# Kernel optimization log

Measured on AMD Instinct MI355X. Metric: run time of the kernel, lower is better.

## Reference

```python
import jax, jax.numpy as jnp
from jax import lax
import numpy as np

S = 2        # scale_factor
K = 5        # upsample_kernel_size
M = 64       # m_channels
C_IN = 128

def setup_inputs() -> dict:
    key = jax.random.key(0)
    k1, k2, k3, k4, k5 = jax.random.split(key, 5)
    B, C, H, W = 8, C_IN, 64, 64
    x = jax.random.normal(k1, (B, C, H, W), dtype=jnp.float32)
    compress_w = jax.random.normal(k2, (M, C, 1, 1), dtype=jnp.float32) * 0.05
    compress_b = jax.random.normal(k3, (M,), dtype=jnp.float32) * 0.05
    n_out = K * K * S * S  # 100
    encoder_w = jax.random.normal(k4, (n_out, M, 3, 3), dtype=jnp.float32) * 0.05
    encoder_b = jax.random.normal(k5, (n_out,), dtype=jnp.float32) * 0.05
    return {"x": x, "compress_w": compress_w, "compress_b": compress_b,
            "encoder_w": encoder_w, "encoder_b": encoder_b}

def _carafe(x, compress_w, compress_b, encoder_w, encoder_b):
    B, C, H, W = x.shape
    k, s = K, S
    nH, nW = s * H, s * W
    # 1x1 compress conv
    m = jnp.einsum('bchw,mc->bmhw', x, compress_w[:, :, 0, 0]) + compress_b[None, :, None, None]
    # 3x3 encoder conv, stride 1, pad 1 (SAME)
    ker = lax.conv_general_dilated(m, encoder_w, window_strides=(1, 1), padding='SAME',
                                   dimension_numbers=('NCHW', 'OIHW', 'NCHW'))
    ker = ker + encoder_b[None, :, None, None]  # (B, k*k*s*s, H, W)
    # PixelShuffle(s): (B, k*k, s, s, H, W) -> (B, k*k, H, s, W, s) -> (B, k*k, nH, nW)
    ker = ker.reshape(B, k * k, s, s, H, W).transpose(0, 1, 4, 2, 5, 3).reshape(B, k * k, nH, nW)
    ker = jax.nn.softmax(ker, axis=1)
    # Unfold(k, stride=1, pad=k//2): stack k*k shifted views, ordering (kh outer, kw inner)
    pad = k // 2
    xp = jnp.pad(x, ((0, 0), (0, 0), (pad, pad), (pad, pad)))
    patches = jnp.stack([xp[:, :, i:i + H, j:j + W] for i in range(k) for j in range(k)],
                        axis=2)  # (B, C, k*k, H, W)
    # nearest upsample by s on spatial dims
    up = jnp.repeat(jnp.repeat(patches, s, axis=3), s, axis=4)  # (B, C, k*k, nH, nW)
    # weighted local sum
    out = jnp.sum(up * ker[:, None, :, :, :], axis=2)  # (B, C, nH, nW)
    return out

def reference(x, compress_w, compress_b, encoder_w, encoder_b):
    return _carafe(x, compress_w, compress_b, encoder_w, encoder_b)
```

## Files before the change

### kernel.cpp

```cpp
#include <hip/hip_runtime.h>
#include <math.h>


typedef __attribute__((ext_vector_type(8))) short short8;
typedef __attribute__((ext_vector_type(4))) float floatx4;
typedef __attribute__((ext_vector_type(2))) float v2f;

__device__ __forceinline__ unsigned short f2bf(float f) {
  union { float f; unsigned int u; } v; v.f = f;
  unsigned int u = v.u + 0x7fffu + ((v.u >> 16) & 1u);
  return (unsigned short)(u >> 16);
}
__device__ __forceinline__ void unpack2(unsigned int u, float& lo, float& hi) {
  union { unsigned int u; float f; } a, b;
  a.u = u << 16; b.u = u & 0xffff0000u;
  lo = a.f; hi = b.f;
}
__device__ __forceinline__ v2f unpack2v(unsigned int u) {
  union { unsigned int u; float f; } a, b;
  a.u = u << 16; b.u = u & 0xffff0000u;
  return (v2f){a.f, b.f};
}

__global__ __launch_bounds__(256) void k_prep_pad(
    const float* __restrict__ x, const float* __restrict__ ew,
    const float* __restrict__ cw, unsigned short* __restrict__ a_prep,
    float* __restrict__ cwT, unsigned short* __restrict__ xpad) {
  const int blk = blockIdx.x;
  if (blk < 1024) {
    const float* xs = x + (size_t)blk * 4096;
    unsigned short* xd = xpad + (size_t)blk * 4896;
    for (int idx = threadIdx.x; idx < 1224; idx += 256) {
      int hp = idx / 18;
      int q = idx - hp * 18;
      int hh = hp - 2;
      int w0 = q * 4 - 2;
      float v0, v1, v2, v3;
      if (hh >= 0 && hh < 64 && w0 >= 0 && w0 + 3 < 64) {
        float4 xv = *(const float4*)&xs[hh * 64 + w0];
        v0 = xv.x; v1 = xv.y; v2 = xv.z; v3 = xv.w;
      } else {
        int base = hh * 64;
        bool hok = (hh >= 0 && hh < 64);
        v0 = (hok && w0 + 0 >= 0 && w0 + 0 < 64) ? xs[base + w0 + 0] : 0.f;
        v1 = (hok && w0 + 1 >= 0 && w0 + 1 < 64) ? xs[base + w0 + 1] : 0.f;
        v2 = (hok && w0 + 2 >= 0 && w0 + 2 < 64) ? xs[base + w0 + 2] : 0.f;
        v3 = (hok && w0 + 3 >= 0 && w0 + 3 < 64) ? xs[base + w0 + 3] : 0.f;
      }
      ushort4 o;
      o.x = f2bf(v0); o.y = f2bf(v1); o.z = f2bf(v2); o.w = f2bf(v3);
      *(ushort4*)&xd[idx * 4] = o;
    }
  } else {
    int idx = (blk - 1024) * 256 + (int)threadIdx.x;
    if (idx < 9 * 128 * 64) {
      int mo = idx & 63;
      int n = (idx >> 6) & 127;
      int tap = idx >> 13;
      float v = (n < 100) ? ew[(n * 64 + mo) * 9 + tap] : 0.f;
      a_prep[idx] = f2bf(v);
    } else {
      int r = idx - 9 * 128 * 64;
      int c = r >> 6, mo = r & 63;
      cwT[c * 64 + mo] = cw[mo * 128 + c];
    }
  }
}

__global__ __launch_bounds__(256) void k_compress(
    const float* __restrict__ x, const float* __restrict__ cwT,
    const float* __restrict__ cb, unsigned short* __restrict__ m_t) {
  __shared__ __align__(16) unsigned short ms[64][72];
  const int b = blockIdx.x >> 6;
  const int h = blockIdx.x & 63;
  const int wv = __builtin_amdgcn_readfirstlane((int)(threadIdx.x >> 6));
  const int lane = (int)(threadIdx.x & 63);
  const int mo0 = wv * 16;

  float acc[16];
#pragma unroll
  for (int k = 0; k < 16; ++k) acc[k] = 0.f;

  const float* xp = x + (((size_t)b * 128) * 64 + h) * 64 + lane;
  const float* wp = cwT + mo0;

#pragma unroll 4
  for (int c = 0; c < 128; ++c) {
    float xv = xp[(size_t)c * 4096];
#pragma unroll
    for (int k = 0; k < 16; ++k)
      acc[k] = fmaf(xv, wp[c * 64 + k], acc[k]);
  }

#pragma unroll
  for (int k = 0; k < 16; ++k) acc[k] += cb[mo0 + k];

#pragma unroll
  for (int k = 0; k < 8; ++k) {
    unsigned int p = ((unsigned int)f2bf(acc[2 * k + 1]) << 16) | f2bf(acc[2 * k]);
    *(unsigned int*)&ms[lane][mo0 + 2 * k] = p;
  }
  __syncthreads();
  const int t = threadIdx.x;
#pragma unroll
  for (int rep = 0; rep < 2; ++rep) {
    int idx = t + rep * 256;
    uint4 v = *(const uint4*)&ms[idx >> 3][(idx & 7) * 8];
    *(uint4*)&m_t[(size_t)blockIdx.x * 4096 + idx * 8] = v;
  }
}

__global__ __launch_bounds__(256) void k_main(
    const unsigned short* __restrict__ m_t, const unsigned short* __restrict__ a_prep,
    const float* __restrict__ eb, const unsigned short* __restrict__ xpad,
    float* __restrict__ out) {
  __shared__ __align__(16) float raw[128 * 66];
  unsigned short* m_s = (unsigned short*)raw;
  unsigned short* wgt_s = (unsigned short*)raw;
  const int b = blockIdx.x >> 6;
  const int h = blockIdx.x & 63;
  const int t = threadIdx.x;

  for (int idx = t; idx < 3 * 64 * 8; idx += 256) {
    int r = idx >> 9;
    int rem = idx & 511;
    int w = rem >> 3, u = rem & 7;
    int hh = h + r - 1;
    uint4 val = make_uint4(0u, 0u, 0u, 0u);
    if (hh >= 0 && hh < 64)
      val = *(const uint4*)&m_t[(((b * 64 + hh) * 64 + w) * 64) + u * 8];
    *(uint4*)&m_s[(r * 64 + w) * 72 + u * 8] = val;
  }
  __syncthreads();

  const int wave = t >> 6, lane = t & 63;
  const int quad = lane >> 4, col = lane & 15;
  const int nbase = wave * 32;

  const floatx4 z4 = {0.f, 0.f, 0.f, 0.f};
  floatx4 acc[2][4];
#pragma unroll
  for (int i = 0; i < 2; ++i)
#pragma unroll
    for (int p = 0; p < 4; ++p) acc[i][p] = z4;

  const short8 z8 = {0, 0, 0, 0, 0, 0, 0, 0};

#pragma unroll
  for (int tap = 0; tap < 9; ++tap) {
    const int dh = tap / 3, dw = tap % 3;
#pragma unroll
    for (int half = 0; half < 2; ++half) {
      const int mo0 = half * 32;
      short8 a0 = *(const short8*)&a_prep[((tap * 128 + nbase + col) * 64) + mo0 + quad * 8];
      short8 a1 = *(const short8*)&a_prep[((tap * 128 + nbase + 16 + col) * 64) + mo0 + quad * 8];
#pragma unroll
      for (int p = 0; p < 4; ++p) {
        int wsrc = p * 16 + col + dw - 1;
        int wc = min(max(wsrc, 0), 63);
        short8 bf = *(const short8*)&m_s[(dh * 64 + wc) * 72 + mo0 + quad * 8];
        if (wsrc < 0 || wsrc > 63) bf = z8;
        acc[0][p] = __builtin_amdgcn_mfma_f32_16x16x32_bf16(a0, bf, acc[0][p], 0, 0, 0);
        acc[1][p] = __builtin_amdgcn_mfma_f32_16x16x32_bf16(a1, bf, acc[1][p], 0, 0, 0);
      }
    }
  }

  __syncthreads();
#pragma unroll
  for (int i = 0; i < 2; ++i)
#pragma unroll
    for (int p = 0; p < 4; ++p)
#pragma unroll
      for (int r = 0; r < 4; ++r)
        raw[(nbase + i * 16 + quad * 4 + r) * 66 + p * 16 + col] = acc[i][p][r];
  __syncthreads();

  const int q = wave;
  float v[25];
  float mx = -1e30f;
#pragma unroll
  for (int kk = 0; kk < 25; ++kk) {
    v[kk] = raw[(kk * 4 + q) * 66 + lane] + eb[kk * 4 + q];
    mx = fmaxf(mx, v[kk]);
  }
  float s = 0.f;
#pragma unroll
  for (int kk = 0; kk < 25; ++kk) {
    v[kk] = __expf(v[kk] - mx);
    s += v[kk];
  }
  float inv = 1.f / s;

  __syncthreads();
  {
    const int ohl = q >> 1;
    const int owp = 2 * lane + (q & 1);
#pragma unroll
    for (int kk = 0; kk < 25; ++kk)
      wgt_s[(ohl * 25 + kk) * 128 + owp] = f2bf(v[kk] * inv);
  }
  __syncthreads();

  const int wg = t & 15;
  const int cg = t >> 4;
  const int w0 = wg * 4;

  for (int chalf = 0; chalf < 2; ++chalf) {
    const int c0 = chalf * 64 + cg * 4;
    const unsigned short* xb =
        xpad + ((size_t)(b * 128 + c0) * 4896) + h * 72 + w0;

    v2f accB[2][4][4];
#pragma unroll
    for (int oh = 0; oh < 2; ++oh)
#pragma unroll
      for (int ch = 0; ch < 4; ++ch)
#pragma unroll
        for (int k = 0; k < 4; ++k) accB[oh][ch][k] = (v2f){0.f, 0.f};

    for (int i = 0; i < 5; ++i) {
      float xr[4][8];
#pragma unroll
      for (int ch = 0; ch < 4; ++ch) {
        uint4 rawv = *(const uint4*)(xb + ch * 4896 + i * 72);
        unpack2(rawv.x, xr[ch][0], xr[ch][1]);
        unpack2(rawv.y, xr[ch][2], xr[ch][3]);
        unpack2(rawv.z, xr[ch][4], xr[ch][5]);
        unpack2(rawv.w, xr[ch][6], xr[ch][7]);
      }
#pragma unroll
      for (int j = 0; j < 5; ++j) {
        const int ij = i * 5 + j;
#pragma unroll
        for (int oh = 0; oh < 2; ++oh) {
          uint4 wr = *(const uint4*)&wgt_s[(oh * 25 + ij) * 128 + w0 * 2];
          v2f wp[4];
          wp[0] = unpack2v(wr.x);
          wp[1] = unpack2v(wr.y);
          wp[2] = unpack2v(wr.z);
          wp[3] = unpack2v(wr.w);
#pragma unroll
          for (int k = 0; k < 4; ++k)
#pragma unroll
            for (int ch = 0; ch < 4; ++ch) {
              float xv = xr[ch][k + j];
              v2f xvv = {xv, xv};
              accB[oh][ch][k] += xvv * wp[k];
            }
        }
      }
    }

#pragma unroll
    for (int ch = 0; ch < 4; ++ch)
#pragma unroll
      for (int oh = 0; oh < 2; ++oh) {
        float* orow =
            out + ((size_t)(b * 128 + c0 + ch) * 128 + (2 * h + oh)) * 128 + w0 * 2;
        float4 f0 = make_float4(accB[oh][ch][0].x, accB[oh][ch][0].y,
                                accB[oh][ch][1].x, accB[oh][ch][1].y);
        float4 f1 = make_float4(accB[oh][ch][2].x, accB[oh][ch][2].y,
                                accB[oh][ch][3].x, accB[oh][ch][3].y);
        *(float4*)orow = f0;
        *(float4*)(orow + 4) = f1;
      }
  }
}

extern "C" void kernel_launch(void* const* d_in, const int* in_sizes, int n_in,
                              void* d_out, int out_size, void* d_ws, size_t ws_size,
                              hipStream_t stream) {
  (void)in_sizes; (void)n_in; (void)out_size; (void)ws_size;
  const float* x  = (const float*)d_in[0];
  const float* cw = (const float*)d_in[1];
  const float* cb = (const float*)d_in[2];
  const float* ew = (const float*)d_in[3];
  const float* eb = (const float*)d_in[4];
  float* out = (float*)d_out;

  char* wsb = (char*)d_ws;
  unsigned short* m_t    = (unsigned short*)(wsb);
  unsigned short* a_prep = (unsigned short*)(wsb + 4194304);
  unsigned short* xpad   = (unsigned short*)(wsb + 4341760);
  float*          cwT    = (float*)(wsb + 14368768);

  k_prep_pad<<<dim3(1344), dim3(256), 0, stream>>>(x, ew, cw, a_prep, cwT, xpad);
  k_compress<<<dim3(512), dim3(256), 0, stream>>>(x, cwT, cb, m_t);
  k_main<<<dim3(512), dim3(256), 0, stream>>>(m_t, a_prep, eb, xpad, out);
}
```

Before: 145.4 us.

## Fuse bf16 padded-x write into compress kernel and widen main kernel to 512 threads

```diff
diff --git a/kernel.cpp b/kernel.cpp
--- a/kernel.cpp
+++ b/kernel.cpp
@@ -23,36 +23,15 @@
 }
 
 __global__ __launch_bounds__(256) void k_prep_pad(
-    const float* __restrict__ x, const float* __restrict__ ew,
-    const float* __restrict__ cw, unsigned short* __restrict__ a_prep,
-    float* __restrict__ cwT, unsigned short* __restrict__ xpad) {
+    const float* __restrict__ ew, const float* __restrict__ cw,
+    unsigned short* __restrict__ a_prep, float* __restrict__ cwT,
+    unsigned short* __restrict__ xpad) {
   const int blk = blockIdx.x;
-  if (blk < 1024) {
-    const float* xs = x + (size_t)blk * 4096;
-    unsigned short* xd = xpad + (size_t)blk * 4896;
-    for (int idx = threadIdx.x; idx < 1224; idx += 256) {
-      int hp = idx / 18;
-      int q = idx - hp * 18;
-      int hh = hp - 2;
-      int w0 = q * 4 - 2;
-      float v0, v1, v2, v3;
-      if (hh >= 0 && hh < 64 && w0 >= 0 && w0 + 3 < 64) {
-        float4 xv = *(const float4*)&xs[hh * 64 + w0];
-        v0 = xv.x; v1 = xv.y; v2 = xv.z; v3 = xv.w;
-      } else {
-        int base = hh * 64;
-        bool hok = (hh >= 0 && hh < 64);
-        v0 = (hok && w0 + 0 >= 0 && w0 + 0 < 64) ? xs[base + w0 + 0] : 0.f;
-        v1 = (hok && w0 + 1 >= 0 && w0 + 1 < 64) ? xs[base + w0 + 1] : 0.f;
-        v2 = (hok && w0 + 2 >= 0 && w0 + 2 < 64) ? xs[base + w0 + 2] : 0.f;
-        v3 = (hok && w0 + 3 >= 0 && w0 + 3 < 64) ? xs[base + w0 + 3] : 0.f;
-      }
-      ushort4 o;
-      o.x = f2bf(v0); o.y = f2bf(v1); o.z = f2bf(v2); o.w = f2bf(v3);
-      *(ushort4*)&xd[idx * 4] = o;
-    }
+  if (blk < 2448) {
+    int idx = blk * 256 + (int)threadIdx.x;
+    *(uint4*)&xpad[(size_t)idx * 8] = make_uint4(0u, 0u, 0u, 0u);
   } else {
-    int idx = (blk - 1024) * 256 + (int)threadIdx.x;
+    int idx = (blk - 2448) * 256 + (int)threadIdx.x;
     if (idx < 9 * 128 * 64) {
       int mo = idx & 63;
       int n = (idx >> 6) & 127;
@@ -69,7 +48,8 @@
 
 __global__ __launch_bounds__(256) void k_compress(
     const float* __restrict__ x, const float* __restrict__ cwT,
-    const float* __restrict__ cb, unsigned short* __restrict__ m_t) {
+    const float* __restrict__ cb, unsigned short* __restrict__ m_t,
+    unsigned short* __restrict__ xpad) {
   __shared__ __align__(16) unsigned short ms[64][72];
   const int b = blockIdx.x >> 6;
   const int h = blockIdx.x & 63;
@@ -83,10 +63,14 @@
 
   const float* xp = x + (((size_t)b * 128) * 64 + h) * 64 + lane;
   const float* wp = cwT + mo0;
+  unsigned short* xpd =
+      xpad + ((size_t)(b * 128) * 4896) + (h + 2) * 72 + 2 + lane;
 
 #pragma unroll 4
   for (int c = 0; c < 128; ++c) {
     float xv = xp[(size_t)c * 4096];
+    if ((c >> 5) == wv)
+      xpd[(size_t)c * 4896] = f2bf(xv);
 #pragma unroll
     for (int k = 0; k < 16; ++k)
       acc[k] = fmaf(xv, wp[c * 64 + k], acc[k]);
@@ -110,7 +94,7 @@
   }
 }
 
-__global__ __launch_bounds__(256) void k_main(
+__global__ __launch_bounds__(512, 4) void k_main(
     const unsigned short* __restrict__ m_t, const unsigned short* __restrict__ a_prep,
     const float* __restrict__ eb, const unsigned short* __restrict__ xpad,
     float* __restrict__ out) {
@@ -121,7 +105,7 @@
   const int h = blockIdx.x & 63;
   const int t = threadIdx.x;
 
-  for (int idx = t; idx < 3 * 64 * 8; idx += 256) {
+  for (int idx = t; idx < 3 * 64 * 8; idx += 512) {
     int r = idx >> 9;
     int rem = idx & 511;
     int w = rem >> 3, u = rem & 7;
@@ -135,14 +119,12 @@
 
   const int wave = t >> 6, lane = t & 63;
   const int quad = lane >> 4, col = lane & 15;
-  const int nbase = wave * 32;
+  const int nbase = wave * 16;
 
   const floatx4 z4 = {0.f, 0.f, 0.f, 0.f};
-  floatx4 acc[2][4];
-#pragma unroll
-  for (int i = 0; i < 2; ++i)
-#pragma unroll
-    for (int p = 0; p < 4; ++p) acc[i][p] = z4;
+  floatx4 acc[4];
+#pragma unroll
+  for (int p = 0; p < 4; ++p) acc[p] = z4;
 
   const short8 z8 = {0, 0, 0, 0, 0, 0, 0, 0};
 
@@ -153,47 +135,46 @@
     for (int half = 0; half < 2; ++half) {
       const int mo0 = half * 32;
       short8 a0 = *(const short8*)&a_prep[((tap * 128 + nbase + col) * 64) + mo0 + quad * 8];
-      short8 a1 = *(const short8*)&a_prep[((tap * 128 + nbase + 16 + col) * 64) + mo0 + quad * 8];
 #pragma unroll
       for (int p = 0; p < 4; ++p) {
         int wsrc = p * 16 + col + dw - 1;
         int wc = min(max(wsrc, 0), 63);
         short8 bf = *(const short8*)&m_s[(dh * 64 + wc) * 72 + mo0 + quad * 8];
         if (wsrc < 0 || wsrc > 63) bf = z8;
-        acc[0][p] = __builtin_amdgcn_mfma_f32_16x16x32_bf16(a0, bf, acc[0][p], 0, 0, 0);
-        acc[1][p] = __builtin_amdgcn_mfma_f32_16x16x32_bf16(a1, bf, acc[1][p], 0, 0, 0);
+        acc[p] = __builtin_amdgcn_mfma_f32_16x16x32_bf16(a0, bf, acc[p], 0, 0, 0);
       }
     }
   }
 
   __syncthreads();
 #pragma unroll
-  for (int i = 0; i < 2; ++i)
-#pragma unroll
-    for (int p = 0; p < 4; ++p)
-#pragma unroll
-      for (int r = 0; r < 4; ++r)
-        raw[(nbase + i * 16 + quad * 4 + r) * 66 + p * 16 + col] = acc[i][p][r];
-  __syncthreads();
-
-  const int q = wave;
+  for (int p = 0; p < 4; ++p)
+#pragma unroll
+    for (int r = 0; r < 4; ++r)
+      raw[(nbase + quad * 4 + r) * 66 + p * 16 + col] = acc[p][r];
+  __syncthreads();
+
   float v[25];
-  float mx = -1e30f;
-#pragma unroll
-  for (int kk = 0; kk < 25; ++kk) {
-    v[kk] = raw[(kk * 4 + q) * 66 + lane] + eb[kk * 4 + q];
-    mx = fmaxf(mx, v[kk]);
-  }
-  float s = 0.f;
-#pragma unroll
-  for (int kk = 0; kk < 25; ++kk) {
-    v[kk] = __expf(v[kk] - mx);
-    s += v[kk];
-  }
-  float inv = 1.f / s;
-
-  __syncthreads();
-  {
+  float inv = 0.f;
+  if (t < 256) {
+    const int q = wave;
+    float mx = -1e30f;
+#pragma unroll
+    for (int kk = 0; kk < 25; ++kk) {
+      v[kk] = raw[(kk * 4 + q) * 66 + lane] + eb[kk * 4 + q];
+      mx = fmaxf(mx, v[kk]);
+    }
+    float s = 0.f;
+#pragma unroll
+    for (int kk = 0; kk < 25; ++kk) {
+      v[kk] = __expf(v[kk] - mx);
+      s += v[kk];
+    }
+    inv = 1.f / s;
+  }
+  __syncthreads();
+  if (t < 256) {
+    const int q = wave;
     const int ohl = q >> 1;
     const int owp = 2 * lane + (q & 1);
 #pragma unroll
@@ -205,67 +186,65 @@
   const int wg = t & 15;
   const int cg = t >> 4;
   const int w0 = wg * 4;
-
-  for (int chalf = 0; chalf < 2; ++chalf) {
-    const int c0 = chalf * 64 + cg * 4;
-    const unsigned short* xb =
-        xpad + ((size_t)(b * 128 + c0) * 4896) + h * 72 + w0;
-
-    v2f accB[2][4][4];
-#pragma unroll
-    for (int oh = 0; oh < 2; ++oh)
-#pragma unroll
-      for (int ch = 0; ch < 4; ++ch)
-#pragma unroll
-        for (int k = 0; k < 4; ++k) accB[oh][ch][k] = (v2f){0.f, 0.f};
-
-    for (int i = 0; i < 5; ++i) {
-      float xr[4][8];
-#pragma unroll
-      for (int ch = 0; ch < 4; ++ch) {
-        uint4 rawv = *(const uint4*)(xb + ch * 4896 + i * 72);
-        unpack2(rawv.x, xr[ch][0], xr[ch][1]);
-        unpack2(rawv.y, xr[ch][2], xr[ch][3]);
-        unpack2(rawv.z, xr[ch][4], xr[ch][5]);
-        unpack2(rawv.w, xr[ch][6], xr[ch][7]);
+  const int c0 = cg * 4;
+
+  const unsigned short* xb =
+      xpad + ((size_t)(b * 128 + c0) * 4896) + h * 72 + w0;
+
+  v2f accB[2][4][4];
+#pragma unroll
+  for (int oh = 0; oh < 2; ++oh)
+#pragma unroll
+    for (int ch = 0; ch < 4; ++ch)
+#pragma unroll
+      for (int k = 0; k < 4; ++k) accB[oh][ch][k] = (v2f){0.f, 0.f};
+
+  for (int i = 0; i < 5; ++i) {
+    float xr[4][8];
+#pragma unroll
+    for (int ch = 0; ch < 4; ++ch) {
+      uint4 rawv = *(const uint4*)(xb + ch * 4896 + i * 72);
+      unpack2(rawv.x, xr[ch][0], xr[ch][1]);
+      unpack2(rawv.y, xr[ch][2], xr[ch][3]);
+      unpack2(rawv.z, xr[ch][4], xr[ch][5]);
+      unpack2(rawv.w, xr[ch][6], xr[ch][7]);
+    }
+#pragma unroll
+    for (int j = 0; j < 5; ++j) {
+      const int ij = i * 5 + j;
+#pragma unroll
+      for (int oh = 0; oh < 2; ++oh) {
+        uint4 wr = *(const uint4*)&wgt_s[(oh * 25 + ij) * 128 + w0 * 2];
+        v2f wp[4];
+        wp[0] = unpack2v(wr.x);
+        wp[1] = unpack2v(wr.y);
+        wp[2] = unpack2v(wr.z);
+        wp[3] = unpack2v(wr.w);
+#pragma unroll
+        for (int k = 0; k < 4; ++k)
+#pragma unroll
+          for (int ch = 0; ch < 4; ++ch) {
+            float xv = xr[ch][k + j];
+            v2f xvv = {xv, xv};
+            accB[oh][ch][k] += xvv * wp[k];
+          }
       }
-#pragma unroll
-      for (int j = 0; j < 5; ++j) {
-        const int ij = i * 5 + j;
-#pragma unroll
-        for (int oh = 0; oh < 2; ++oh) {
-          uint4 wr = *(const uint4*)&wgt_s[(oh * 25 + ij) * 128 + w0 * 2];
-          v2f wp[4];
-          wp[0] = unpack2v(wr.x);
-          wp[1] = unpack2v(wr.y);
-          wp[2] = unpack2v(wr.z);
-          wp[3] = unpack2v(wr.w);
-#pragma unroll
-          for (int k = 0; k < 4; ++k)
-#pragma unroll
-            for (int ch = 0; ch < 4; ++ch) {
-              float xv = xr[ch][k + j];
-              v2f xvv = {xv, xv};
-              accB[oh][ch][k] += xvv * wp[k];
-            }
-        }
-      }
-    }
-
-#pragma unroll
-    for (int ch = 0; ch < 4; ++ch)
-#pragma unroll
-      for (int oh = 0; oh < 2; ++oh) {
-        float* orow =
-            out + ((size_t)(b * 128 + c0 + ch) * 128 + (2 * h + oh)) * 128 + w0 * 2;
-        float4 f0 = make_float4(accB[oh][ch][0].x, accB[oh][ch][0].y,
-                                accB[oh][ch][1].x, accB[oh][ch][1].y);
-        float4 f1 = make_float4(accB[oh][ch][2].x, accB[oh][ch][2].y,
-                                accB[oh][ch][3].x, accB[oh][ch][3].y);
-        *(float4*)orow = f0;
-        *(float4*)(orow + 4) = f1;
-      }
-  }
+    }
+  }
+
+#pragma unroll
+  for (int ch = 0; ch < 4; ++ch)
+#pragma unroll
+    for (int oh = 0; oh < 2; ++oh) {
+      float* orow =
+          out + ((size_t)(b * 128 + c0 + ch) * 128 + (2 * h + oh)) * 128 + w0 * 2;
+      float4 f0 = make_float4(accB[oh][ch][0].x, accB[oh][ch][0].y,
+                              accB[oh][ch][1].x, accB[oh][ch][1].y);
+      float4 f1 = make_float4(accB[oh][ch][2].x, accB[oh][ch][2].y,
+                              accB[oh][ch][3].x, accB[oh][ch][3].y);
+      *(float4*)orow = f0;
+      *(float4*)(orow + 4) = f1;
+    }
 }
 
 extern "C" void kernel_launch(void* const* d_in, const int* in_sizes, int n_in,
@@ -285,7 +264,7 @@
   unsigned short* xpad   = (unsigned short*)(wsb + 4341760);
   float*          cwT    = (float*)(wsb + 14368768);
 
-  k_prep_pad<<<dim3(1344), dim3(256), 0, stream>>>(x, ew, cw, a_prep, cwT, xpad);
-  k_compress<<<dim3(512), dim3(256), 0, stream>>>(x, cwT, cb, m_t);
-  k_main<<<dim3(512), dim3(256), 0, stream>>>(m_t, a_prep, eb, xpad, out);
-}
+  k_prep_pad<<<dim3(2768), dim3(256), 0, stream>>>(ew, cw, a_prep, cwT, xpad);
+  k_compress<<<dim3(512), dim3(256), 0, stream>>>(x, cwT, cb, m_t, xpad);
+  k_main<<<dim3(512), dim3(512), 0, stream>>>(m_t, a_prep, eb, xpad, out);
+}
```

New measurement: 153.5 us. 1.06x slower.
